# Optimization experiments

Measured on AMD Instinct MI355X. Metric: run time of the kernel, lower is better.

Reference implementation:

```python
import jax, jax.numpy as jnp
import numpy as np

B, L, S, H = 8, 128, 160, 768      # batch, words, wordpieces, bert hidden
T, CD = 16, 50                      # max chars per word, char embed/lstm dim
WV, WD = 50000, 100                 # word vocab, word embed dim
CV = 128                            # char vocab
NEG = -1e30


def _run_lstm(x, w_ih, w_hh, b):
    # x: [N, T, D] -> hidden states [N, T, Hc]; torch LSTM gate order i,f,g,o
    N = x.shape[0]
    Hc = w_hh.shape[1]
    def step(carry, xt):
        h, c = carry
        g = xt @ w_ih.T + h @ w_hh.T + b
        i, f, gg, o = jnp.split(g, 4, axis=-1)
        c = jax.nn.sigmoid(f) * c + jax.nn.sigmoid(i) * jnp.tanh(gg)
        h = jax.nn.sigmoid(o) * jnp.tanh(c)
        return (h, c), h
    init = (jnp.zeros((N, Hc), x.dtype), jnp.zeros((N, Hc), x.dtype))
    _, hs = jax.lax.scan(step, init, jnp.swapaxes(x, 0, 1))
    return jnp.swapaxes(hs, 0, 1)


def setup_inputs() -> dict:
    key = jax.random.key(0)
    ks = jax.random.split(key, 14)
    sc = 1.0 / np.sqrt(CD)
    return {
        "bert_emb": jax.random.normal(ks[0], (B, S, H), jnp.float32),
        "pieces2word": jax.random.randint(ks[1], (B, L, S), 0, 2, jnp.int32),
        "word_ids": jax.random.randint(ks[2], (B, L), 0, WV),
        "char_ids": jax.random.randint(ks[3], (B, L, T), 0, CV),
        "char_count": jax.random.randint(ks[4], (B, L), 0, T, jnp.int32),
        "token_masks_char": jax.random.randint(ks[5], (B, L, T), 0, 2, jnp.int32),
        "word_table": jax.random.normal(ks[6], (WV, WD), jnp.float32) * 0.02,
        "char_table": jax.random.normal(ks[7], (CV, CD), jnp.float32) * 0.02,
        "w_ih_f": jax.random.uniform(ks[8], (4 * CD, CD), jnp.float32, -sc, sc),
        "w_hh_f": jax.random.uniform(ks[9], (4 * CD, CD), jnp.float32, -sc, sc),
        "b_f": jax.random.uniform(ks[10], (4 * CD,), jnp.float32, -sc, sc),
        "w_ih_b": jax.random.uniform(ks[11], (4 * CD, CD), jnp.float32, -sc, sc),
        "w_hh_b": jax.random.uniform(ks[12], (4 * CD, CD), jnp.float32, -sc, sc),
        "b_b": jax.random.uniform(ks[13], (4 * CD,), jnp.float32, -sc, sc),
    }


def reference(bert_emb, pieces2word, word_ids, char_ids, char_count,
              token_masks_char, word_table, char_table,
              w_ih_f, w_hh_f, b_f, w_ih_b, w_hh_b, b_b):
    cls_embedding = bert_emb[:, 0]                      # [B, H]
    # piece -> word max pooling (masked fill with global min, then max)
    min_value = jax.lax.stop_gradient(jnp.min(bert_emb))
    expanded = jnp.where(pieces2word[:, :, :, None] != 0,
                         bert_emb[:, None, :, :], min_value)  # [B, L, S, H]
    word_reps = jnp.max(expanded, axis=2)               # [B, L, H]

    # word embedding lookup (emb_dropout is identity in eval)
    word_embed = word_table[word_ids]                   # [B, L, WD]

    # char biLSTM
    N = B * L
    lengths = jnp.maximum(char_count.reshape(N), 1)     # char_count[==0] = 1
    x = char_table[char_ids.reshape(N, T)]              # [N, T, CD]
    h_fwd = _run_lstm(x, w_ih_f, w_hh_f, b_f)           # [N, T, CD]
    # reverse each sequence by its true length (packed-sequence semantics)
    t = jnp.arange(T)
    rev_idx = lengths[:, None] - 1 - t[None, :]         # [N, T]
    valid = (rev_idx >= 0).astype(x.dtype)[:, :, None]
    gidx = jnp.clip(rev_idx, 0, T - 1)[:, :, None]
    x_rev = jnp.take_along_axis(x, gidx, axis=1) * valid
    h_rev = _run_lstm(x_rev, w_ih_b, w_hh_b, b_b)
    h_bwd = jnp.take_along_axis(h_rev, gidx, axis=1) * valid  # un-reverse + zero pad
    char_h = jnp.concatenate([h_fwd, h_bwd], axis=-1).reshape(B, L, T, 2 * CD)

    # combine(..., 'max'): additive -1e30 mask, max over chars, zero all-masked
    m = jnp.where(token_masks_char[:, :, :, None] == 0, NEG, 0.0).astype(char_h.dtype)
    h_token_char = jnp.max(m + char_h, axis=2)
    h_token_char = jnp.where(h_token_char == NEG, 0.0, h_token_char)  # [B, L, 2CD]

    embeds = jnp.concatenate([word_reps, word_embed, h_token_char], axis=-1)
    return embeds, cls_embedding
```

## Files before the change

kernel.cpp:

```cpp
#include <hip/hip_runtime.h>

#define B_   8
#define L_   128
#define S_   160
#define H_   768
#define T_   16
#define CD_  50
#define WD_  100
#define NGATE 200
#define NEGV (-1e30f)
#define FMAXV 3.402823466e+38f
#define NELEM (B_ * S_ * H_)

typedef short  s16x8 __attribute__((ext_vector_type(8)));
typedef float  f32x4 __attribute__((ext_vector_type(4)));

__device__ __forceinline__ unsigned short f2bf(float f) {
    unsigned u = __float_as_uint(f);
    u = (u + 0x7FFFu + ((u >> 16) & 1u)) >> 16;
    return (unsigned short)u;
}
__device__ __forceinline__ float sigm(float x) {
    return __fdividef(1.f, 1.f + __expf(-x));
}
__device__ __forceinline__ float tanh_fast(float x) {
    float a = fabsf(x);
    float e = __expf(-2.f * a);
    float t = __fdividef(1.f - e, 1.f + e);
    return copysignf(t, x);
}
__device__ __forceinline__ float4 fmax4(float4 a, float4 b) {
    return make_float4(fmaxf(a.x, b.x), fmaxf(a.y, b.y), fmaxf(a.z, b.z), fmaxf(a.w, b.w));
}

#define GSTRIDE 213

struct LstmS {
    s16x8 xall[T_][128];
    s16x8 hbuf[128];
    float gbuf[16][GSTRIDE];
    int   slen[16], smask[16];
};
struct WordS {
    int list[S_ + 4];
    int cnt;
    float red[256];
};
#define SMEM_BYTES 48704

__device__ void lstm_body(int unit, char* smem,
        const int* __restrict__ char_ids, const int* __restrict__ char_count,
        const int* __restrict__ tok_mask, const float* __restrict__ char_table,
        const float* __restrict__ w_ih_f, const float* __restrict__ w_hh_f,
        const float* __restrict__ b_f,
        const float* __restrict__ w_ih_b, const float* __restrict__ w_hh_b,
        const float* __restrict__ b_b,
        float* __restrict__ out) {
    LstmS& sh = *(LstmS*)smem;
    const int dir  = unit >> 6;
    const int grp  = unit & 63;
    const int tid  = threadIdx.x;
    const int lane = tid & 63;
    const int wv   = tid >> 6;

    if (tid < 16) {
        int n = grp * 16 + tid;
        int c = char_count[n];
        sh.slen[tid] = (c > 0) ? c : 1;
        int mb = 0;
        for (int t = 0; t < T_; ++t) mb |= (tok_mask[n * T_ + t] != 0) << t;
        sh.smask[tid] = mb;
    }
    if (tid < 128) { s16x8 z = {0,0,0,0,0,0,0,0}; sh.hbuf[tid] = z; }

    const float* WI = dir ? w_ih_b : w_ih_f;
    const float* WH = dir ? w_hh_b : w_hh_f;
    const float* BV = dir ? b_b    : b_f;
    const int cnt = (wv == 0) ? 4 : 3;
    int   colj[4];
    float bv[4];
    s16x8 bf[4][4];
#pragma unroll
    for (int i = 0; i < 4; ++i) {
        int nt = (i < 3) ? (wv + 4 * i) : 12;
        int j  = nt * 16 + (lane & 15);
        bool jv = (i < cnt) && (j < NGATE);
        colj[i] = j;
        bv[i]   = jv ? BV[j] : 0.f;
        const float* wi = WI + j * CD_;
        const float* wh = WH + j * CD_;
#pragma unroll
        for (int kt = 0; kt < 4; ++kt) {
            int kst = kt * 32 + (lane >> 4) * 8;
            s16x8 fr = {0,0,0,0,0,0,0,0};
#pragma unroll
            for (int e = 0; e < 8; ++e) {
                int k = kst + e;
                float v = 0.f;
                if (jv) {
                    if (k < 64) { if (k < CD_) v = wi[k]; }
                    else        { int k2 = k - 64; if (k2 < CD_) v = wh[k2]; }
                }
                fr[e] = (short)f2bf(v);
            }
            bf[i][kt] = fr;
        }
    }
    __syncthreads();

    for (int idx = tid; idx < T_ * 128; idx += 256) {
        int t = idx >> 7;
        int u = idx & 127;
        int g = u >> 4, s = u & 15;
        int st = dir ? (sh.slen[s] - 1 - t) : t;
        s16x8 fr = {0,0,0,0,0,0,0,0};
        if (st >= 0) {
            int cidv = char_ids[(grp * 16 + s) * T_ + st];
            const float* row = char_table + cidv * CD_;
            int kbase = g * 8;
#pragma unroll
            for (int e = 0; e < 8; ++e) {
                int k = kbase + e;
                if (k < CD_) fr[e] = (short)f2bf(row[k]);
            }
        }
        sh.xall[t][u] = fr;
    }

    const int laneofs = ((lane >> 4) << 4) + (lane & 15);
    const int srow    = (lane >> 4) * 4;

#define SLOT_DECL(K, UU) \
    const int  uu##K = (UU); \
    const bool v##K  = uu##K < 800; \
    const int  s##K  = v##K ? (uu##K / 50) : 0; \
    const int  c##K  = uu##K - s##K * 50; \
    const int  hofs##K = ((c##K >> 3) * 16 + s##K) * 8 + (c##K & 7); \
    int  sl##K = 1, sm##K = 0; \
    float cst##K = 0.f, mr##K = NEGV;
    SLOT_DECL(0, tid)
    SLOT_DECL(1, tid + 256)
    SLOT_DECL(2, tid + 512)
    SLOT_DECL(3, tid + 768)
    sl0 = sh.slen[s0]; sm0 = sh.smask[s0];
    sl1 = sh.slen[s1]; sm1 = sh.smask[s1];
    sl2 = sh.slen[s2]; sm2 = sh.smask[s2];
    sl3 = sh.slen[s3]; sm3 = sh.smask[s3];
    __syncthreads();

#pragma unroll 1
    for (int t = 0; t < T_; ++t) {
        const s16x8* xb = sh.xall[t];
        s16x8 a0 = xb[laneofs];
        s16x8 a1 = xb[64 + laneofs];
        s16x8 a2 = sh.hbuf[laneofs];
        s16x8 a3 = sh.hbuf[64 + laneofs];
#pragma unroll
        for (int i = 0; i < 4; ++i) {
            f32x4 d = {bv[i], bv[i], bv[i], bv[i]};
            d = __builtin_amdgcn_mfma_f32_16x16x32_bf16(a0, bf[i][0], d, 0, 0, 0);
            d = __builtin_amdgcn_mfma_f32_16x16x32_bf16(a1, bf[i][1], d, 0, 0, 0);
            d = __builtin_amdgcn_mfma_f32_16x16x32_bf16(a2, bf[i][2], d, 0, 0, 0);
            d = __builtin_amdgcn_mfma_f32_16x16x32_bf16(a3, bf[i][3], d, 0, 0, 0);
            if (i < cnt) {
                int g = colj[i];
#pragma unroll
                for (int r = 0; r < 4; ++r) sh.gbuf[srow + r][g] = d[r];
            }
        }
        __syncthreads();

#define UPD(K) if (v##K) { \
    float gi = sh.gbuf[s##K][c##K]; \
    float gf = sh.gbuf[s##K][c##K + 50]; \
    float gg = sh.gbuf[s##K][c##K + 100]; \
    float go = sh.gbuf[s##K][c##K + 150]; \
    float cc = sigm(gf) * cst##K + sigm(gi) * tanh_fast(gg); \
    float h  = sigm(go) * tanh_fast(cc); \
    cst##K = cc; \
    ((unsigned short*)sh.hbuf)[hofs##K] = f2bf(h); \
    int tt = dir ? (sl##K - 1 - t) : t; \
    if (tt >= 0 && ((sm##K >> tt) & 1)) mr##K = fmaxf(mr##K, h); }
        UPD(0) UPD(1) UPD(2) UPD(3)
        __syncthreads();
    }

#define OUTW(K) if (v##K) { \
    float m = mr##K; \
    if (dir && (sm##K >> sl##K)) m = fmaxf(m, 0.f); \
    if (m == NEGV) m = 0.f; \
    out[(size_t)(grp * 16 + s##K) * 968 + 868 + dir * CD_ + c##K] = m; }
    OUTW(0) OUTW(1) OUTW(2) OUTW(3)
}

__device__ void word_body(int bl, char* smem,
        const float* __restrict__ bert, const int* __restrict__ p2w,
        const int* __restrict__ word_ids, const float* __restrict__ word_table,
        float* __restrict__ out) {
    WordS& sh = *(WordS*)smem;
    int b = bl >> 7;
    int l = bl & 127;
    int tid = threadIdx.x;

    if (tid == 0) sh.cnt = 0;
    __syncthreads();
    if (tid < S_) {
        if (p2w[bl * S_ + tid]) {
            int p = atomicAdd(&sh.cnt, 1);
            sh.list[p] = tid;
        }
    }
    __syncthreads();
    int n = sh.cnt;

    float* orow = out + (size_t)bl * 968;

    if (n > 0) {
        if (tid < ((4 - (n & 3)) & 3)) sh.list[n + tid] = sh.list[0];
        __syncthreads();
        int n4 = (n + 3) & ~3;
        if (tid < 192) {
            const float4* bb = (const float4*)(bert + (size_t)b * S_ * H_) + tid;
            float4 m = make_float4(-FMAXV, -FMAXV, -FMAXV, -FMAXV);
            for (int i = 0; i < n4; i += 4) {
                int s0 = sh.list[i], s1 = sh.list[i + 1], s2 = sh.list[i + 2], s3 = sh.list[i + 3];
                float4 v0 = bb[(size_t)s0 * 192];
                float4 v1 = bb[(size_t)s1 * 192];
                float4 v2 = bb[(size_t)s2 * 192];
                float4 v3 = bb[(size_t)s3 * 192];
                m = fmax4(m, fmax4(fmax4(v0, v1), fmax4(v2, v3)));
            }
            ((float4*)orow)[tid] = m;
        } else {
            int j = tid - 192;
            int wid = word_ids[bl];
            orow[768 + j] = word_table[(size_t)wid * WD_ + j];
            if (j < WD_ - 64) orow[768 + 64 + j] = word_table[(size_t)wid * WD_ + 64 + j];
        }
    } else {
        float mv = FMAXV;
        const float4* x4 = (const float4*)bert;
        for (int i = tid; i < NELEM / 4; i += 256) {
            float4 v = x4[i];
            mv = fminf(mv, fminf(fminf(v.x, v.y), fminf(v.z, v.w)));
        }
        sh.red[tid] = mv;
        __syncthreads();
        for (int o = 128; o > 0; o >>= 1) {
            if (tid < o) sh.red[tid] = fminf(sh.red[tid], sh.red[tid + o]);
            __syncthreads();
        }
        float g = sh.red[0];
        if (tid < 192) {
            ((float4*)orow)[tid] = make_float4(g, g, g, g);
        } else {
            int j = tid - 192;
            int wid = word_ids[bl];
            orow[768 + j] = word_table[(size_t)wid * WD_ + j];
            if (j < WD_ - 64) orow[768 + 64 + j] = word_table[(size_t)wid * WD_ + 64 + j];
        }
    }

    if (l == 0 && tid < 192) {
        const float4* c4 = (const float4*)(bert + (size_t)b * S_ * H_);
        float4* co = (float4*)(out + (size_t)B_ * L_ * 968 + (size_t)b * H_);
        co[tid] = c4[tid];
    }
}

__global__ __launch_bounds__(256, 3) void kmega(
        const float* __restrict__ bert, const int* __restrict__ p2w,
        const int* __restrict__ word_ids, const int* __restrict__ char_ids,
        const int* __restrict__ char_count, const int* __restrict__ tok_mask,
        const float* __restrict__ word_table, const float* __restrict__ char_table,
        const float* __restrict__ w_ih_f, const float* __restrict__ w_hh_f,
        const float* __restrict__ b_f,
        const float* __restrict__ w_ih_b, const float* __restrict__ w_hh_b,
        const float* __restrict__ b_b,
        float* __restrict__ out) {
    __shared__ __align__(16) char smem[SMEM_BYTES];
    int bid = blockIdx.x;
    if (bid < 128) {
        lstm_body(bid, smem, char_ids, char_count, tok_mask, char_table,
                  w_ih_f, w_hh_f, b_f, w_ih_b, w_hh_b, b_b, out);
    } else {
        word_body(bid - 128, smem, bert, p2w, word_ids, word_table, out);
    }
}

extern "C" void kernel_launch(void* const* d_in, const int* in_sizes, int n_in,
                              void* d_out, int out_size, void* d_ws, size_t ws_size,
                              hipStream_t stream) {
    const float* bert       = (const float*)d_in[0];
    const int*   p2w        = (const int*)d_in[1];
    const int*   word_ids   = (const int*)d_in[2];
    const int*   char_ids   = (const int*)d_in[3];
    const int*   char_count = (const int*)d_in[4];
    const int*   tok_mask   = (const int*)d_in[5];
    const float* word_table = (const float*)d_in[6];
    const float* char_table = (const float*)d_in[7];
    const float* w_ih_f = (const float*)d_in[8];
    const float* w_hh_f = (const float*)d_in[9];
    const float* b_f    = (const float*)d_in[10];
    const float* w_ih_b = (const float*)d_in[11];
    const float* w_hh_b = (const float*)d_in[12];
    const float* b_b    = (const float*)d_in[13];

    float* out = (float*)d_out;

    kmega<<<128 + B_ * L_, 256, 0, stream>>>(bert, p2w, word_ids, char_ids, char_count, tok_mask,
                                             word_table, char_table,
                                             w_ih_f, w_hh_f, b_f, w_ih_b, w_hh_b, b_b, out);
}
```

Before: 44.97 us.

## Keep LSTM gates in registers via permuted weight columns and lane shuffles

Reorders the weight columns so that each lane's MFMA output tile holds the i/f/g/o gates for one (sequence, channel) pair, after a 4-lane shuffle transpose. This removes the shared-memory gate buffer and one of the two barriers per timestep. The hidden state is double-buffered so writes for the next step do not race with reads of the current one. Separately, the word max-pool loop is unrolled to 8 gathered loads per iteration to get more memory-level parallelism. Cost: extra shuffle instructions, and activation math is now computed by all lanes, including padded channels.

```diff
diff --git a/kernel.cpp b/kernel.cpp
--- a/kernel.cpp
+++ b/kernel.cpp
@@ -33,20 +33,17 @@
     return make_float4(fmaxf(a.x, b.x), fmaxf(a.y, b.y), fmaxf(a.z, b.z), fmaxf(a.w, b.w));
 }
 
-#define GSTRIDE 213
-
 struct LstmS {
     s16x8 xall[T_][128];
-    s16x8 hbuf[128];
-    float gbuf[16][GSTRIDE];
+    s16x8 hbuf[2][128];
     int   slen[16], smask[16];
 };
 struct WordS {
-    int list[S_ + 4];
+    int list[S_ + 8];
     int cnt;
     float red[256];
 };
-#define SMEM_BYTES 48704
+#define SMEM_BYTES 37120
 
 __device__ void lstm_body(int unit, char* smem,
         const int* __restrict__ char_ids, const int* __restrict__ char_count,
@@ -71,27 +68,38 @@
         for (int t = 0; t < T_; ++t) mb |= (tok_mask[n * T_ + t] != 0) << t;
         sh.smask[tid] = mb;
     }
-    if (tid < 128) { s16x8 z = {0,0,0,0,0,0,0,0}; sh.hbuf[tid] = z; }
+    { s16x8 z = {0,0,0,0,0,0,0,0};
+      if (tid < 128) sh.hbuf[0][tid] = z; else sh.hbuf[1][tid - 128] = z; }
+
+    const int m   = lane & 3;
+    const int k2  = (lane >> 2) & 3;
+    const int q   = lane >> 4;
+    const int sstar = q * 4 + m;
 
     const float* WI = dir ? w_ih_b : w_ih_f;
     const float* WH = dir ? w_hh_b : w_hh_f;
     const float* BV = dir ? b_b    : b_f;
     const int cnt = (wv == 0) ? 4 : 3;
-    int   colj[4];
+    int   ccol[4];
+    int   cvld[4];
+    int   hofs[4];
     float bv[4];
     s16x8 bf[4][4];
 #pragma unroll
     for (int i = 0; i < 4; ++i) {
         int nt = (i < 3) ? (wv + 4 * i) : 12;
-        int j  = nt * 16 + (lane & 15);
-        bool jv = (i < cnt) && (j < NGATE);
-        colj[i] = j;
-        bv[i]   = jv ? BV[j] : 0.f;
-        const float* wi = WI + j * CD_;
-        const float* wh = WH + j * CD_;
+        int c  = nt * 4 + k2;
+        int jv = (i < cnt) && (c < 50);
+        ccol[i] = c;
+        cvld[i] = jv;
+        hofs[i] = ((c >> 3) * 16 + sstar) * 8 + (c & 7);
+        int orow = m * 50 + c;
+        bv[i] = jv ? BV[orow] : 0.f;
+        const float* wi = WI + orow * CD_;
+        const float* wh = WH + orow * CD_;
 #pragma unroll
         for (int kt = 0; kt < 4; ++kt) {
-            int kst = kt * 32 + (lane >> 4) * 8;
+            int kst = kt * 32 + q * 8;
             s16x8 fr = {0,0,0,0,0,0,0,0};
 #pragma unroll
             for (int e = 0; e < 8; ++e) {
@@ -99,7 +107,7 @@
                 float v = 0.f;
                 if (jv) {
                     if (k < 64) { if (k < CD_) v = wi[k]; }
-                    else        { int k2 = k - 64; if (k2 < CD_) v = wh[k2]; }
+                    else        { int kk = k - 64; if (kk < CD_) v = wh[kk]; }
                 }
                 fr[e] = (short)f2bf(v);
             }
@@ -127,69 +135,89 @@
         sh.xall[t][u] = fr;
     }
 
-    const int laneofs = ((lane >> 4) << 4) + (lane & 15);
-    const int srow    = (lane >> 4) * 4;
-
-#define SLOT_DECL(K, UU) \
-    const int  uu##K = (UU); \
-    const bool v##K  = uu##K < 800; \
-    const int  s##K  = v##K ? (uu##K / 50) : 0; \
-    const int  c##K  = uu##K - s##K * 50; \
-    const int  hofs##K = ((c##K >> 3) * 16 + s##K) * 8 + (c##K & 7); \
-    int  sl##K = 1, sm##K = 0; \
-    float cst##K = 0.f, mr##K = NEGV;
-    SLOT_DECL(0, tid)
-    SLOT_DECL(1, tid + 256)
-    SLOT_DECL(2, tid + 512)
-    SLOT_DECL(3, tid + 768)
-    sl0 = sh.slen[s0]; sm0 = sh.smask[s0];
-    sl1 = sh.slen[s1]; sm1 = sh.smask[s1];
-    sl2 = sh.slen[s2]; sm2 = sh.smask[s2];
-    sl3 = sh.slen[s3]; sm3 = sh.smask[s3];
+    const int laneofs = (q << 4) + (lane & 15);
+    const int sl_s = sh.slen[sstar];
+    const int sm_s = sh.smask[sstar];
+
+    float cst0 = 0.f, cst1 = 0.f, cst2 = 0.f, cst3 = 0.f;
+    float mr0 = NEGV, mr1 = NEGV, mr2 = NEGV, mr3 = NEGV;
+    const bool m0 = (lane & 1) != 0;
+    const bool m1 = (lane & 2) != 0;
+
     __syncthreads();
+
+#define TRUPD(I, D) { \
+    float v0 = (D)[0], v1 = (D)[1], v2 = (D)[2], v3 = (D)[3]; \
+    float s10 = __shfl_xor(v0, 1), s11 = __shfl_xor(v1, 1); \
+    float s12 = __shfl_xor(v2, 1), s13 = __shfl_xor(v3, 1); \
+    float A0 = m0 ? s11 : v0; \
+    float A1 = m0 ? v1 : s10; \
+    float A2 = m0 ? s13 : v2; \
+    float A3 = m0 ? v3 : s12; \
+    float s20 = __shfl_xor(A0, 2), s21 = __shfl_xor(A1, 2); \
+    float s22 = __shfl_xor(A2, 2), s23 = __shfl_xor(A3, 2); \
+    float gi = m1 ? s22 : A0; \
+    float gf = m1 ? s23 : A1; \
+    float gg = m1 ? A2 : s20; \
+    float go = m1 ? A3 : s21; \
+    float cc = sigm(gf) * cst##I + sigm(gi) * tanh_fast(gg); \
+    float h  = sigm(go) * tanh_fast(cc); \
+    if (cvld[I]) { \
+        cst##I = cc; \
+        hw[hofs[I]] = f2bf(h); \
+        int tt = dir ? (sl_s - 1 - t) : t; \
+        if (tt >= 0 && ((sm_s >> tt) & 1)) mr##I = fmaxf(mr##I, h); \
+    } }
 
 #pragma unroll 1
     for (int t = 0; t < T_; ++t) {
+        const int cur = t & 1, nxt = cur ^ 1;
+        unsigned short* hw = (unsigned short*)&sh.hbuf[nxt][0];
         const s16x8* xb = sh.xall[t];
         s16x8 a0 = xb[laneofs];
         s16x8 a1 = xb[64 + laneofs];
-        s16x8 a2 = sh.hbuf[laneofs];
-        s16x8 a3 = sh.hbuf[64 + laneofs];
-#pragma unroll
-        for (int i = 0; i < 4; ++i) {
-            f32x4 d = {bv[i], bv[i], bv[i], bv[i]};
-            d = __builtin_amdgcn_mfma_f32_16x16x32_bf16(a0, bf[i][0], d, 0, 0, 0);
-            d = __builtin_amdgcn_mfma_f32_16x16x32_bf16(a1, bf[i][1], d, 0, 0, 0);
-            d = __builtin_amdgcn_mfma_f32_16x16x32_bf16(a2, bf[i][2], d, 0, 0, 0);
-            d = __builtin_amdgcn_mfma_f32_16x16x32_bf16(a3, bf[i][3], d, 0, 0, 0);
-            if (i < cnt) {
-                int g = colj[i];
-#pragma unroll
-                for (int r = 0; r < 4; ++r) sh.gbuf[srow + r][g] = d[r];
+        s16x8 a2 = sh.hbuf[cur][laneofs];
+        s16x8 a3 = sh.hbuf[cur][64 + laneofs];
+
+        {
+            f32x4 d0 = {bv[0], bv[0], bv[0], bv[0]};
+            f32x4 d1 = {bv[1], bv[1], bv[1], bv[1]};
+            d0 = __builtin_amdgcn_mfma_f32_16x16x32_bf16(a0, bf[0][0], d0, 0, 0, 0);
+            d1 = __builtin_amdgcn_mfma_f32_16x16x32_bf16(a0, bf[1][0], d1, 0, 0, 0);
+            d0 = __builtin_amdgcn_mfma_f32_16x16x32_bf16(a1, bf[0][1], d0, 0, 0, 0);
+            d1 = __builtin_amdgcn_mfma_f32_16x16x32_bf16(a1, bf[1][1], d1, 0, 0, 0);
+            d0 = __builtin_amdgcn_mfma_f32_16x16x32_bf16(a2, bf[0][2], d0, 0, 0, 0);
+            d1 = __builtin_amdgcn_mfma_f32_16x16x32_bf16(a2, bf[1][2], d1, 0, 0, 0);
+            d0 = __builtin_amdgcn_mfma_f32_16x16x32_bf16(a3, bf[0][3], d0, 0, 0, 0);
+            d1 = __builtin_amdgcn_mfma_f32_16x16x32_bf16(a3, bf[1][3], d1, 0, 0, 0);
+            TRUPD(0, d0)
+            TRUPD(1, d1)
+        }
+        {
+            f32x4 d2 = {bv[2], bv[2], bv[2], bv[2]};
+            d2 = __builtin_amdgcn_mfma_f32_16x16x32_bf16(a0, bf[2][0], d2, 0, 0, 0);
+            d2 = __builtin_amdgcn_mfma_f32_16x16x32_bf16(a1, bf[2][1], d2, 0, 0, 0);
+            d2 = __builtin_amdgcn_mfma_f32_16x16x32_bf16(a2, bf[2][2], d2, 0, 0, 0);
+            d2 = __builtin_amdgcn_mfma_f32_16x16x32_bf16(a3, bf[2][3], d2, 0, 0, 0);
+            TRUPD(2, d2)
+            if (cnt == 4) {
+                f32x4 d3 = {bv[3], bv[3], bv[3], bv[3]};
+                d3 = __builtin_amdgcn_mfma_f32_16x16x32_bf16(a0, bf[3][0], d3, 0, 0, 0);
+                d3 = __builtin_amdgcn_mfma_f32_16x16x32_bf16(a1, bf[3][1], d3, 0, 0, 0);
+                d3 = __builtin_amdgcn_mfma_f32_16x16x32_bf16(a2, bf[3][2], d3, 0, 0, 0);
+                d3 = __builtin_amdgcn_mfma_f32_16x16x32_bf16(a3, bf[3][3], d3, 0, 0, 0);
+                TRUPD(3, d3)
             }
         }
         __syncthreads();
-
-#define UPD(K) if (v##K) { \
-    float gi = sh.gbuf[s##K][c##K]; \
-    float gf = sh.gbuf[s##K][c##K + 50]; \
-    float gg = sh.gbuf[s##K][c##K + 100]; \
-    float go = sh.gbuf[s##K][c##K + 150]; \
-    float cc = sigm(gf) * cst##K + sigm(gi) * tanh_fast(gg); \
-    float h  = sigm(go) * tanh_fast(cc); \
-    cst##K = cc; \
-    ((unsigned short*)sh.hbuf)[hofs##K] = f2bf(h); \
-    int tt = dir ? (sl##K - 1 - t) : t; \
-    if (tt >= 0 && ((sm##K >> tt) & 1)) mr##K = fmaxf(mr##K, h); }
-        UPD(0) UPD(1) UPD(2) UPD(3)
-        __syncthreads();
-    }
-
-#define OUTW(K) if (v##K) { \
-    float m = mr##K; \
-    if (dir && (sm##K >> sl##K)) m = fmaxf(m, 0.f); \
-    if (m == NEGV) m = 0.f; \
-    out[(size_t)(grp * 16 + s##K) * 968 + 868 + dir * CD_ + c##K] = m; }
+    }
+
+    float* ob = out + (size_t)(grp * 16 + sstar) * 968 + 868 + dir * CD_;
+#define OUTW(I) if (cvld[I]) { \
+    float mm = mr##I; \
+    if (dir && (sm_s >> sl_s)) mm = fmaxf(mm, 0.f); \
+    if (mm == NEGV) mm = 0.f; \
+    ob[ccol[I]] = mm; }
     OUTW(0) OUTW(1) OUTW(2) OUTW(3)
 }
 
@@ -216,21 +244,25 @@
     float* orow = out + (size_t)bl * 968;
 
     if (n > 0) {
-        if (tid < ((4 - (n & 3)) & 3)) sh.list[n + tid] = sh.list[0];
+        if (tid < ((8 - (n & 7)) & 7)) sh.list[n + tid] = sh.list[0];
         __syncthreads();
-        int n4 = (n + 3) & ~3;
+        int n8 = (n + 7) & ~7;
         if (tid < 192) {
             const float4* bb = (const float4*)(bert + (size_t)b * S_ * H_) + tid;
-            float4 m = make_float4(-FMAXV, -FMAXV, -FMAXV, -FMAXV);
-            for (int i = 0; i < n4; i += 4) {
-                int s0 = sh.list[i], s1 = sh.list[i + 1], s2 = sh.list[i + 2], s3 = sh.list[i + 3];
-                float4 v0 = bb[(size_t)s0 * 192];
-                float4 v1 = bb[(size_t)s1 * 192];
-                float4 v2 = bb[(size_t)s2 * 192];
-                float4 v3 = bb[(size_t)s3 * 192];
-                m = fmax4(m, fmax4(fmax4(v0, v1), fmax4(v2, v3)));
+            float4 mx = make_float4(-FMAXV, -FMAXV, -FMAXV, -FMAXV);
+            for (int i = 0; i < n8; i += 8) {
+                float4 v0 = bb[(size_t)sh.list[i]     * 192];
+                float4 v1 = bb[(size_t)sh.list[i + 1] * 192];
+                float4 v2 = bb[(size_t)sh.list[i + 2] * 192];
+                float4 v3 = bb[(size_t)sh.list[i + 3] * 192];
+                float4 v4 = bb[(size_t)sh.list[i + 4] * 192];
+                float4 v5 = bb[(size_t)sh.list[i + 5] * 192];
+                float4 v6 = bb[(size_t)sh.list[i + 6] * 192];
+                float4 v7 = bb[(size_t)sh.list[i + 7] * 192];
+                mx = fmax4(mx, fmax4(fmax4(fmax4(v0, v1), fmax4(v2, v3)),
+                                     fmax4(fmax4(v4, v5), fmax4(v6, v7))));
             }
-            ((float4*)orow)[tid] = m;
+            ((float4*)orow)[tid] = mx;
         } else {
             int j = tid - 192;
             int wid = word_ids[bl];
```

Measured after the change: 44.95 us. No clear change (-0.1%).
